# Optimization experiments

Hardware: AMD Instinct MI355X
Metric: run time of the kernel (lower is better)

The kernel has to match this reference:

```python
import jax, jax.numpy as jnp
import numpy as np

B = 8
A = 3
LEVEL_HW = [(200, 304), (100, 152), (50, 76), (25, 38), (13, 19)]
LEVEL_SIZES = [A * h * w for h, w in LEVEL_HW]  # anchors per level
N_TOTAL = sum(LEVEL_SIZES)                      # 242991
IMG_H, IMG_W = 800.0, 1216.0
PRE_NMS_TOP_N = 2000
POST_NMS_TOP_N = 100
NMS_THRESH = 0.7
MIN_SIZE = 1e-3
BBOX_XFORM_CLIP = float(np.log(1000.0 / 16.0))
NEG = -1e30


def setup_inputs() -> dict:
    key = jax.random.key(0)
    ks = jax.random.split(key, 2 * len(LEVEL_HW) + 3)
    inp = {}
    for i, (h, w) in enumerate(LEVEL_HW):
        inp[f"cls{i}"] = jax.random.normal(ks[2 * i], (B, A, h, w), dtype=jnp.float32)
        inp[f"box{i}"] = jax.random.normal(ks[2 * i + 1], (B, 4 * A, h, w), dtype=jnp.float32) * 0.5
    kc, kw, _ = ks[-3], ks[-2], ks[-1]
    c = jax.random.uniform(kc, (N_TOTAL, 2), dtype=jnp.float32) * jnp.array([IMG_W, IMG_H], jnp.float32)
    wh = 16.0 + jax.random.uniform(kw, (N_TOTAL, 2), dtype=jnp.float32) * 240.0
    inp["anchors"] = jnp.concatenate([c - 0.5 * wh, c + 0.5 * wh], axis=-1)  # x1y1x2y2
    return inp


def _permute_flatten(p, C):
    # [N, A*C, H, W] -> [N, H*W*A, C]  (matches permute_and_flatten)
    n, ac, h, w = p.shape
    a = ac // C
    return p.reshape(n, a, C, h, w).transpose(0, 3, 4, 1, 2).reshape(n, -1, C)


def _decode(deltas, anchors):
    wa = anchors[:, 2] - anchors[:, 0]
    ha = anchors[:, 3] - anchors[:, 1]
    cxa = anchors[:, 0] + 0.5 * wa
    cya = anchors[:, 1] + 0.5 * ha
    dx, dy = deltas[..., 0], deltas[..., 1]
    dw = jnp.minimum(deltas[..., 2], BBOX_XFORM_CLIP)
    dh = jnp.minimum(deltas[..., 3], BBOX_XFORM_CLIP)
    cx = dx * wa + cxa
    cy = dy * ha + cya
    pw = jnp.exp(dw) * wa
    ph = jnp.exp(dh) * ha
    return jnp.stack([cx - 0.5 * pw, cy - 0.5 * ph, cx + 0.5 * pw, cy + 0.5 * ph], axis=-1)


def _nms_single(boxes, scores, lvl, valid):
    # batched_nms: offset boxes by level so cross-level boxes never overlap
    off = lvl.astype(boxes.dtype)[:, None] * (max(IMG_H, IMG_W) + 1.0)
    b0 = boxes + off
    s0 = jnp.where(valid, scores, NEG)  # small-box removal -> impossible to pick
    order = jnp.argsort(-s0)
    b = b0[order]
    s = s0[order]
    areas = (b[:, 2] - b[:, 0]) * (b[:, 3] - b[:, 1])
    suppressed0 = s <= NEG / 2
    idx_range = jnp.arange(s.shape[0])

    def step(suppressed, _):
        avail = jnp.where(suppressed, NEG, s)
        i = jnp.argmax(avail)
        ok = avail[i] > NEG / 2
        bi = b[i]
        xx1 = jnp.maximum(b[:, 0], bi[0])
        yy1 = jnp.maximum(b[:, 1], bi[1])
        xx2 = jnp.minimum(b[:, 2], bi[2])
        yy2 = jnp.minimum(b[:, 3], bi[3])
        inter = jnp.maximum(xx2 - xx1, 0.0) * jnp.maximum(yy2 - yy1, 0.0)
        union = areas + areas[i] - inter
        iou = jnp.where(union > 0, inter / union, 0.0)
        sup_new = suppressed | (iou > NMS_THRESH) | (idx_range == i)
        return jnp.where(ok, sup_new, suppressed), (jnp.where(ok, order[i], 0), ok)

    _, (sel, selv) = jax.lax.scan(step, suppressed0, None, length=POST_NMS_TOP_N)
    out_boxes = jnp.where(selv[:, None], boxes[sel], 0.0)
    out_scores = jnp.where(selv, scores[sel], 0.0)
    return out_boxes, out_scores


def reference(cls0, cls1, cls2, cls3, cls4, box0, box1, box2, box3, box4, anchors):
    cls_levels = [cls0, cls1, cls2, cls3, cls4]
    box_levels = [box0, box1, box2, box3, box4]
    pred_class = jnp.concatenate([_permute_flatten(c, 1) for c in cls_levels], axis=1)  # [B,N,1]
    deltas = jnp.concatenate([_permute_flatten(b, 4) for b in box_levels], axis=1)      # [B,N,4]
    proposals = _decode(deltas, anchors)                                               # [B,N,4]
    scores = pred_class[..., 0]                                                        # [B,N]

    # per-level top-k; replicates the original's cumulative k = min(k, num_anchor)
    keep, lvl = [], []
    k, off = PRE_NMS_TOP_N, 0
    for li, n in enumerate(LEVEL_SIZES):
        k = min(k, n)
        _, idx = jax.lax.top_k(scores[:, off:off + n], k)
        keep.append(idx + off)
        lvl.append(jnp.full((k,), li, dtype=jnp.int32))
        off += n
    keep = jnp.concatenate(keep, axis=1)   # [B,K]
    lvl = jnp.concatenate(lvl)             # [K]

    prop = jnp.take_along_axis(proposals, keep[..., None], axis=1)  # [B,K,4]
    sc = jnp.take_along_axis(scores, keep, axis=1)                  # [B,K]
    prop = jnp.stack([
        jnp.clip(prop[..., 0], 0.0, IMG_W), jnp.clip(prop[..., 1], 0.0, IMG_H),
        jnp.clip(prop[..., 2], 0.0, IMG_W), jnp.clip(prop[..., 3], 0.0, IMG_H)], axis=-1)
    valid = ((prop[..., 2] - prop[..., 0]) >= MIN_SIZE) & ((prop[..., 3] - prop[..., 1]) >= MIN_SIZE)
    boxes_out, scores_out = jax.vmap(lambda bx, s, v: _nms_single(bx, s, lvl, v))(prop, sc, valid)
    return boxes_out, scores_out  # [B,100,4], [B,100]
```

## Files before the change

### kernel.cpp

```cpp
#include <hip/hip_runtime.h>
#include <cstdint>

#define NTOT 242991
#define BATCH 8
#define KTOT 8741
#define CAP 8192
#define NBIN 4096
#define CSTR 16
#define MEMTOT 1943928
#define SLICE 256
#define RSTR 9
#define BCAP 2048
#define NB2 2048

__device__ __forceinline__ int level_of(int n) {
    if (n < 182400) return 0;
    if (n < 228000) return 1;
    if (n < 239400) return 2;
    if (n < 242250) return 3;
    return 4;
}

__device__ __forceinline__ void locate(int n, int& l, int& H, int& W, int& loc) {
    if (n < 182400)      { l = 0; H = 200; W = 304; loc = n; }
    else if (n < 228000) { l = 1; H = 100; W = 152; loc = n - 182400; }
    else if (n < 239400) { l = 2; H = 50;  W = 76;  loc = n - 228000; }
    else if (n < 242250) { l = 3; H = 25;  W = 38;  loc = n - 239400; }
    else                 { l = 4; H = 13;  W = 19;  loc = n - 242250; }
}

__device__ __forceinline__ int classify_bl(int x) {
    int l, HW;
    if (x < 1459200)      { l = 0; HW = 60800; }
    else if (x < 1824000) { l = 1; HW = 15200; x -= 1459200; }
    else if (x < 1915200) { l = 2; HW = 3800;  x -= 1824000; }
    else if (x < 1938000) { l = 3; HW = 950;   x -= 1915200; }
    else                  { l = 4; HW = 247;   x -= 1938000; }
    return (x / (3 * HW)) * 5 + l;
}

__device__ __forceinline__ void mem_decompose(int x, int& b, int& n, int& bl) {
    int HW, off, l;
    if (x < 1459200)      { l = 0; HW = 60800; off = 0; }
    else if (x < 1824000) { l = 1; HW = 15200; off = 182400; x -= 1459200; }
    else if (x < 1915200) { l = 2; HW = 3800;  off = 228000; x -= 1824000; }
    else if (x < 1938000) { l = 3; HW = 950;   off = 239400; x -= 1915200; }
    else                  { l = 4; HW = 247;   off = 242250; x -= 1938000; }
    int seg = 3 * HW;
    b = x / seg; int r = x - b * seg;
    int a = r / HW, pix = r - a * HW;
    n = off + pix * 3 + a;
    bl = b * 5 + l;
}

__device__ __forceinline__ float read_cls(int gid, const float* c0, const float* c1,
                                          const float* c2, const float* c3, const float* c4) {
    return (gid < 1459200) ? c0[gid] :
           (gid < 1824000) ? c1[gid - 1459200] :
           (gid < 1915200) ? c2[gid - 1824000] :
           (gid < 1938000) ? c3[gid - 1915200] : c4[gid - 1938000];
}

__device__ __forceinline__ uint32_t suffix_scan_1024(uint32_t g, uint32_t* lds16, int t) {
    int lane = t & 63, wid = t >> 6;
    uint32_t v = g;
#pragma unroll
    for (int o = 1; o < 64; o <<= 1) {
        uint32_t oth = __shfl_down(v, o, 64);
        if (lane + o < 64) v += oth;
    }
    if (lane == 0) lds16[wid] = v;
    __syncthreads();
    uint32_t w = 0;
    for (int q = wid + 1; q < 16; q++) w += lds16[q];
    __syncthreads();
    return v + w;
}

__device__ __forceinline__ unsigned long long suffix_scan64(unsigned long long g,
                                                            unsigned long long* lds64, int t) {
    int lane = t & 63, wid = t >> 6;
    unsigned long long v = g;
#pragma unroll
    for (int o = 1; o < 64; o <<= 1) {
        unsigned long long oth = __shfl_down(v, o, 64);
        if (lane + o < 64) v += oth;
    }
    if (lane == 0) lds64[wid] = v;
    __syncthreads();
    unsigned long long w = 0;
    for (int q = wid + 1; q < 16; q++) w += lds64[q];
    __syncthreads();
    return v + w;
}

__device__ __forceinline__ uint32_t prefix_scan_1024(uint32_t g, uint32_t* lds16, int t) {
    int lane = t & 63, wid = t >> 6;
    uint32_t v = g;
#pragma unroll
    for (int o = 1; o < 64; o <<= 1) {
        uint32_t oth = __shfl_up(v, o, 64);
        if (lane >= o) v += oth;
    }
    if (lane == 63) lds16[wid] = v;
    __syncthreads();
    uint32_t w = 0;
    for (int q = 0; q < wid; q++) w += lds16[q];
    __syncthreads();
    return v + w;
}

__device__ __forceinline__ bool iou_hit(float bx1, float by1, float bx2, float by2, float ca,
                                        float4 sv) {
    float xx1 = fmaxf(bx1, sv.x), yy1 = fmaxf(by1, sv.y);
    float xx2 = fminf(bx2, sv.z), yy2 = fminf(by2, sv.w);
    float inter = fmaxf(xx2 - xx1, 0.f) * fmaxf(yy2 - yy1, 0.f);
    float sa = (sv.z - sv.x) * (sv.w - sv.y);
    float un = ca + sa - inter;
    return (un > 0.f) && (inter / un > 0.7f);
}

__global__ __launch_bounds__(1024)
void k_keys(const float* __restrict__ c0, const float* __restrict__ c1,
            const float* __restrict__ c2, const float* __restrict__ c3,
            const float* __restrict__ c4, uint32_t* __restrict__ hist) {
    int t = threadIdx.x;
    int base = blockIdx.x * 1024;
    int gid = base + t;
    bool in = gid < MEMTOT;
    __shared__ uint32_t lh[NBIN];

    int bl = 0, b, n;
    uint32_t u = 0;
    if (in) {
        mem_decompose(gid, b, n, bl);
        float sv = read_cls(gid, c0, c1, c2, c3, c4);
        u = __float_as_uint(sv);
        u ^= (u >> 31) ? 0xFFFFFFFFu : 0x80000000u;
    }
    int blf = classify_bl(base);
    int bll = classify_bl(min(base + 1023, MEMTOT - 1));
    if (blf == bll) {
        for (int j = t; j < NBIN; j += 1024) lh[j] = 0u;
        __syncthreads();
        if (in) atomicAdd(&lh[u >> 20], 1u);
        __syncthreads();
        uint32_t* gh = hist + (size_t)blf * NBIN;
        for (int j = t; j < NBIN; j += 1024) {
            uint32_t v = lh[j];
            if (v) atomicAdd(&gh[j], v);
        }
    } else {
        if (in) atomicAdd(&hist[(size_t)bl * NBIN + (u >> 20)], 1u);
    }
}

__global__ void k_bins(const uint32_t* __restrict__ hist, int* __restrict__ binT,
                       int* __restrict__ rrem) {
    int bl = blockIdx.x;
    const uint32_t* h = hist + (size_t)bl * NBIN;
    int l = bl % 5;
    uint32_t k = (l == 4) ? 741u : 2000u;
    __shared__ uint32_t ts[256];
    __shared__ uint32_t sb[256];
    int t = threadIdx.x;
    uint32_t hh[16];
#pragma unroll
    for (int i = 0; i < 16; i++) hh[i] = h[t * 16 + i];
    uint32_t s = 0;
#pragma unroll
    for (int i = 0; i < 16; i++) s += hh[i];
    ts[t] = s; sb[t] = s;
    __syncthreads();
    for (int d = 1; d < 256; d <<= 1) {
// ... 82 lines not shown
            if (p < CAP) {
                cand_n[(size_t)bl * CAP + p] = (uint32_t)n;
                cand_u[(size_t)bl * CAP + p] = u;
            }
        }
    }
}

__global__ __launch_bounds__(1024)
void k_select(const uint32_t* __restrict__ cand_n, const uint32_t* __restrict__ cand_u,
              const uint32_t* __restrict__ cand_cnt, const int* __restrict__ rrem,
              uint32_t* __restrict__ keep_n, uint32_t* __restrict__ keep_u,
              uint32_t* __restrict__ keep_cnt) {
    int bl = blockIdx.x;
    int b = bl / 5, l = bl % 5;
    int C = (int)min(cand_cnt[bl * CSTR], (uint32_t)CAP);
    int r = rrem[bl];
    const uint32_t* cdn = cand_n + (size_t)bl * CAP;
    const uint32_t* cdu = cand_u + (size_t)bl * CAP;
    __shared__ uint32_t hist_l[2048];
    __shared__ uint32_t lds16[16];
    __shared__ unsigned long long pref_sh;
    __shared__ uint32_t kk_sh;
    int t = threadIdx.x;
    if (t == 0) { pref_sh = 0ull; kk_sh = (uint32_t)r; }
    unsigned long long maskAcc = 0ull;
    const int shifts[5] = {41, 30, 19, 8, 0};
    const uint32_t masks[5] = {0x7FFu, 0x7FFu, 0x7FFu, 0x7FFu, 0xFFu};
    __syncthreads();
    for (int p = 0; p < 5; p++) {
        int shift = shifts[p];
        uint32_t msk = masks[p];
        for (int j = t; j < 2048; j += 1024) hist_l[j] = 0u;
        __syncthreads();
        unsigned long long pref = pref_sh;
        uint32_t kk = kk_sh;
        for (int i = t; i < C; i += 1024) {
            unsigned long long key =
                ((unsigned long long)cdu[i] << 32) | (uint32_t)(~cdn[i]);
            if ((key & maskAcc) == pref)
                atomicAdd(&hist_l[(uint32_t)(key >> shift) & msk], 1u);
        }
        __syncthreads();
        uint32_t g = hist_l[2 * t] + hist_l[2 * t + 1];
        uint32_t inc = suffix_scan_1024(g, lds16, t);
        uint32_t excl = inc - g;
        if (excl < kk && inc >= kk) {
            uint32_t hh1 = hist_l[2 * t + 1];
            uint32_t digit, rem;
            if (excl + hh1 >= kk) { digit = 2 * t + 1; rem = kk - excl; }
            else { digit = 2 * t; rem = kk - (excl + hh1); }
            pref_sh = pref | ((unsigned long long)digit << shift);
            kk_sh = rem;
        }
        __syncthreads();
        maskAcc |= (unsigned long long)msk << shift;
    }
    unsigned long long Tk = pref_sh;
    __syncthreads();
    int lane = t & 63;
    for (int i0 = 0; i0 < C; i0 += 1024) {
        int i = i0 + t;
        bool in = i < C;
        uint32_t n = in ? cdn[i] : 0u;
        uint32_t u = in ? cdu[i] : 0u;
        unsigned long long key = in ?
            (((unsigned long long)u << 32) | (uint32_t)(~n)) : 0ull;
        bool pr = in && ((key & maskAcc) >= Tk);
        unsigned long long mk = __ballot(pr);
        if (mk) {
            int leader = __ffsll(mk) - 1;
            uint32_t bs = 0;
            if (lane == leader) bs = atomicAdd(&keep_cnt[bl * CSTR], (uint32_t)__popcll(mk));
            bs = __shfl(bs, leader, 64);
            if (pr) {
                uint32_t p = (uint32_t)(b * KTOT + l * 2000) + bs +
                             (uint32_t)__popcll(mk & ((1ull << lane) - 1ull));
                keep_n[p] = n; keep_u[p] = u;
            }
        }
    }
}

__global__ __launch_bounds__(1024)
void k_prep(const float* __restrict__ b0, const float* __restrict__ b1,
            const float* __restrict__ b2, const float* __restrict__ b3,
            const float* __restrict__ b4, const float* __restrict__ anchors,
            const uint32_t* __restrict__ keep_n, const uint32_t* __restrict__ keep_u,
            unsigned long long* __restrict__ skey, float4* __restrict__ sbox,
            uint32_t* __restrict__ nb_start, uint32_t* __restrict__ nb_cnt,
            uint32_t* __restrict__ nb_id, uint32_t* __restrict__ nbcnt) {
    int b = blockIdx.x, t = threadIdx.x;
    __shared__ uint32_t shist_l[NBIN];
    __shared__ uint32_t scur_l[NBIN];
    __shared__ unsigned long long lds64[16];
    for (int j = t; j < NBIN; j += 1024) shist_l[j] = 0u;
    __syncthreads();

    float4 bx[9]; unsigned long long ky[9];
#pragma unroll
    for (int e = 0; e < 9; e++) {
        int i = t + e * 1024;
        ky[e] = 0ull; bx[e] = make_float4(0.f, 0.f, 0.f, 0.f);
        if (i < KTOT) {
            int gid = b * KTOT + i;
            int n = (int)keep_n[gid];
            uint32_t u = keep_u[gid];
            int l, H, W, loc; locate(n, l, H, W, loc);
            int a = loc % 3, hw = loc / 3;
            int w = hw % W, h = hw / W;
            const float* bp = (l == 0) ? b0 : (l == 1) ? b1 : (l == 2) ? b2
                              : (l == 3) ? b3 : b4;
            int HW = H * W;
            int base = ((b * 12 + a * 4) * H + h) * W + w;
            float dx = bp[base], dy = bp[base + HW];
            float dw = bp[base + 2 * HW], dh = bp[base + 3 * HW];
            float ax1 = anchors[4 * n], ay1 = anchors[4 * n + 1];
            float ax2 = anchors[4 * n + 2], ay2 = anchors[4 * n + 3];
            float wa = ax2 - ax1, ha = ay2 - ay1;
            float cxa = ax1 + 0.5f * wa, cya = ay1 + 0.5f * ha;
            const float CLIPV = 4.135166556742356f;
            dw = fminf(dw, CLIPV); dh = fminf(dh, CLIPV);
            float cx = dx * wa + cxa, cy = dy * ha + cya;
            float pw = expf(dw) * wa, ph = expf(dh) * ha;
            float x1 = cx - 0.5f * pw, y1 = cy - 0.5f * ph;
            float x2 = cx + 0.5f * pw, y2 = cy + 0.5f * ph;
            x1 = fminf(fmaxf(x1, 0.f), 1216.f); x2 = fminf(fmaxf(x2, 0.f), 1216.f);
            y1 = fminf(fmaxf(y1, 0.f), 800.f);  y2 = fminf(fmaxf(y2, 0.f), 800.f);
            bool valid = ((x2 - x1) >= 1e-3f) && ((y2 - y1) >= 1e-3f);
            if (valid) {
                float off = (float)l * 1217.0f;
                bx[e] = make_float4(x1 + off, y1 + off, x2 + off, y2 + off);
                ky[e] = ((unsigned long long)u << 32) | (uint32_t)(~n);
                atomicAdd(&shist_l[u >> 20], 1u);
            }
        }
    }
    __syncthreads();
    uint32_t h0 = shist_l[4 * t], h1 = shist_l[4 * t + 1],
             h2 = shist_l[4 * t + 2], h3 = shist_l[4 * t + 3];
#define PK(c) ((unsigned long long)(c) | ((unsigned long long)((c) > 0u) << 32))
    unsigned long long g = PK(h0) + PK(h1) + PK(h2) + PK(h3);
    unsigned long long inc = suffix_scan64(g, lds64, t);
    unsigned long long acc = inc - g;
    uint32_t* NBS = nb_start + (size_t)b * NBIN;
    uint32_t* NBC = nb_cnt + (size_t)b * NBIN;
    uint32_t* NBI = nb_id + (size_t)b * NBIN;
#define EMIT(q, cq) { int bin = 4 * t + (q); uint32_t st = (uint32_t)acc;            \
                      uint32_t fp = (uint32_t)(acc >> 32);                           \
                      scur_l[bin] = st;                                              \
                      if (cq) { NBS[fp] = st; NBC[fp] = cq; NBI[fp] = (uint32_t)bin; } \
                      acc += PK(cq); }
    EMIT(3, h3) EMIT(2, h2) EMIT(1, h1) EMIT(0, h0)
#undef EMIT
#undef PK
    if (t == 0) nbcnt[b] = (uint32_t)(inc >> 32);
    __syncthreads();
#pragma unroll
    for (int e = 0; e < 9; e++) {
        if (ky[e] != 0ull) {
            uint32_t bucket = (uint32_t)(ky[e] >> 52);
            uint32_t p = atomicAdd(&scur_l[bucket], 1u);
            skey[(size_t)b * KTOT + p] = ky[e];
            sbox[(size_t)b * KTOT + p] = bx[e];
        }
    }
}

__global__ __launch_bounds__(1024)
void k_scan(const unsigned long long* __restrict__ skey, const float4* __restrict__ sbox,
            const uint32_t* __restrict__ nb_start, const uint32_t* __restrict__ nb_cnt,
            const uint32_t* __restrict__ nb_id, const uint32_t* __restrict__ nbcnt,
            float* __restrict__ out) {
    int b = blockIdx.x, t = threadIdx.x, lane = t & 63, wid = t >> 6;
    const unsigned long long* SK = skey + (size_t)b * KTOT;
    const float4* BXs = sbox + (size_t)b * KTOT;
    const uint32_t* NBS = nb_start + (size_t)b * NBIN;
    const uint32_t* NBC = nb_cnt + (size_t)b * NBIN;
    const uint32_t* NBI = nb_id + (size_t)b * NBIN;

    __shared__ unsigned long long k_l[BCAP];
    __shared__ unsigned short p_l[BCAP];
    __shared__ uint32_t hist2[NB2];
    __shared__ uint32_t scur2[NB2];
    __shared__ unsigned char rnk[NBIN];
    __shared__ float box_x[SLICE], box_y[SLICE], box_z[SLICE], box_w[SLICE];
    __shared__ uint32_t rows[SLICE * RSTR];
    __shared__ float4 sel_l[100];
    __shared__ uint32_t sup[SLICE / 32];
    __shared__ uint32_t lds16[16];
    __shared__ uint32_t picks_sh;
    __shared__ unsigned long long gmax_sh;
    __shared__ uint32_t jpos_sh;
    __shared__ unsigned long long wred[16];

    uint32_t nbc = nbcnt[b];
    uint32_t picks = 0;
    uint32_t e = 0;
    while (e < nbc && picks < 100u) {
        uint32_t bstart = NBS[e];
        uint32_t total = 0, nb = 0;
        while (e + nb < nbc && nb < 8u) {
            uint32_t c = NBC[e + nb];
            if (nb > 0u && total + c > (uint32_t)BCAP) break;
            total += c; nb++;
            if (total >= (uint32_t)BCAP) break;
        }

        if (total <= (uint32_t)BCAP) {
            if (t < (int)nb) rnk[NBI[e + t]] = (unsigned char)t;
            for (int j2 = t; j2 < NB2; j2 += 1024) hist2[j2] = 0u;
            __syncthreads();
            unsigned long long k0 = 0ull, k1 = 0ull;
            uint32_t bin0 = 0xFFFFFFFFu, bin1 = 0xFFFFFFFFu;
            if ((uint32_t)t < total) {
                k0 = SK[bstart + (uint32_t)t];
                bin0 = ((uint32_t)rnk[(uint32_t)(k0 >> 52)] << 8) |
                       (255u - (uint32_t)((k0 >> 44) & 0xFFull));
                atomicAdd(&hist2[bin0], 1u);
            }
            if ((uint32_t)t + 1024u < total) {
                k1 = SK[bstart + (uint32_t)t + 1024u];
                bin1 = ((uint32_t)rnk[(uint32_t)(k1 >> 52)] << 8) |
                       (255u - (uint32_t)((k1 >> 44) & 0xFFull));
                atomicAdd(&hist2[bin1], 1u);
            }
            __syncthreads();
            uint32_t h0 = hist2[2 * t], h1 = hist2[2 * t + 1];
            uint32_t inc = prefix_scan_1024(h0 + h1, lds16, t);
            uint32_t excl = inc - (h0 + h1);
            scur2[2 * t] = excl; scur2[2 * t + 1] = excl + h0;
            __syncthreads();
            if (bin0 != 0xFFFFFFFFu) {
                uint32_t pos = atomicAdd(&scur2[bin0], 1u);
                k_l[pos] = k0; p_l[pos] = (unsigned short)(bstart + (uint32_t)t);
            }
            if (bin1 != 0xFFFFFFFFu) {
                uint32_t pos = atomicAdd(&scur2[bin1], 1u);
                k_l[pos] = k1; p_l[pos] = (unsigned short)(bstart + (uint32_t)t + 1024u);
            }
            __syncthreads();
#pragma unroll
            for (int q = 0; q < 2; q++) {
                uint32_t bin = 2 * (uint32_t)t + (uint32_t)q;
                uint32_t c = hist2[bin];
                if (c > 1u) {
                    uint32_t st = scur2[bin] - c;
                    for (uint32_t a = st + 1; a < st + c; a++) {
                        unsigned long long kv = k_l[a]; unsigned short pv = p_l[a];
                        uint32_t w2 = a;
                        while (w2 > st && k_l[w2 - 1] < kv) {
                            k_l[w2] = k_l[w2 - 1]; p_l[w2] = p_l[w2 - 1]; w2--;
                        }
                        k_l[w2] = kv; p_l[w2] = pv;
                    }
                }
            }
            __syncthreads();

            for (uint32_t s0 = 0; s0 < total && picks < 100u; s0 += SLICE) {
                uint32_t sl = min((uint32_t)SLICE, total - s0);
                if (t < SLICE) {
                    if (t < (int)sl) {
                        float4 cb = BXs[p_l[s0 + t]];
                        box_x[t] = cb.x; box_y[t] = cb.y; box_z[t] = cb.z; box_w[t] = cb.w;
                    } else {
                        box_x[t] = 0.f; box_y[t] = 0.f; box_z[t] = 0.f; box_w[t] = 0.f;
                    }
                }
                if (t < SLICE / 32) sup[t] = 0u;
                __syncthreads();
                if (picks > 0u && t < (int)sl) {
                    float bx1 = box_x[t], by1 = box_y[t], bx2 = box_z[t], by2 = box_w[t];
                    float ca = (bx2 - bx1) * (by2 - by1);
                    bool hit = false;
                    uint32_t s = 0;
                    for (; s + 4 <= picks; s += 4) {
                        float4 v0 = sel_l[s], v1 = sel_l[s + 1], v2 = sel_l[s + 2],
                               v3 = sel_l[s + 3];
                        hit = hit | iou_hit(bx1, by1, bx2, by2, ca, v0)
                                  | iou_hit(bx1, by1, bx2, by2, ca, v1)
                                  | iou_hit(bx1, by1, bx2, by2, ca, v2)
                                  | iou_hit(bx1, by1, bx2, by2, ca, v3);
                    }
                    for (; s < picks; s++) hit = hit | iou_hit(bx1, by1, bx2, by2, ca, sel_l[s]);
                    if (hit) atomicOr(&sup[t >> 5], 1u << (t & 31));
                }
                for (uint32_t widx = t; widx < SLICE * 8; widx += 1024) {
                    uint32_t i = widx & (SLICE - 1);
                    uint32_t wq = widx >> 8;
                    float bx1 = box_x[i], by1 = box_y[i], bx2 = box_z[i], by2 = box_w[i];
                    float ai = (bx2 - bx1) * (by2 - by1);
                    uint32_t jbase = wq * 32u, bits = 0u;
#pragma unroll
                    for (uint32_t qq = 0; qq < 32u; qq++) {
                        uint32_t jj = jbase + qq;
                        float jx1 = box_x[jj], jy1 = box_y[jj],
                              jx2 = box_z[jj], jy2 = box_w[jj];
                        float xx1 = fmaxf(bx1, jx1), yy1 = fmaxf(by1, jy1);
                        float xx2 = fminf(bx2, jx2), yy2 = fminf(by2, jy2);
                        float inter = fmaxf(xx2 - xx1, 0.f) * fmaxf(yy2 - yy1, 0.f);
                        float aj = (jx2 - jx1) * (jy2 - jy1);
                        float un = ai + aj - inter;
                        bool sp = (jj > i) && (un > 0.f) && (inter / un > 0.7f);
                        bits |= ((uint32_t)sp) << qq;
                    }
                    rows[i * RSTR + wq] = bits;
                }
                __syncthreads();
                if (wid == 0) {
                    uint32_t myw = (lane < SLICE / 32) ? sup[lane] : 0u;
                    uint32_t pk = picks;
                    for (uint32_t i = 0; i < sl && pk < 100u; i++) {
                        uint32_t wv = __shfl(myw, (int)(i >> 5), 64);
                        if (!((wv >> (i & 31)) & 1u)) {
                            if (lane < SLICE / 32) myw |= rows[i * RSTR + lane];
                            if (lane == 0) {
                                float4 cb = make_float4(box_x[i], box_y[i], box_z[i], box_w[i]);
                                sel_l[pk] = cb;
                                unsigned long long mkey = k_l[s0 + i];
                                uint32_t n = ~(uint32_t)(mkey & 0xFFFFFFFFull);
                                float off = (float)level_of((int)n) * 1217.0f;
                                float* ob = out + ((size_t)b * 100 + pk) * 4;
                                ob[0] = cb.x - off; ob[1] = cb.y - off;
                                ob[2] = cb.z - off; ob[3] = cb.w - off;
                                uint32_t uu = (uint32_t)(mkey >> 32);
                                uint32_t sb2 = (uu & 0x80000000u) ? (uu ^ 0x80000000u) : ~uu;
                                out[3200 + b * 100 + pk] = __uint_as_float(sb2);
                            }
                            pk++;
                        }
                    }
                    if (lane == 0) picks_sh = pk;
                }
                __syncthreads();
                picks = picks_sh;
            }
        } else {
            unsigned long long last = 0ull;
            bool first = true;
            for (uint32_t done = 0; done < total && picks < 100u; done++) {
                unsigned long long lbest = 0ull;
                uint32_t jbest = 0;
                for (uint32_t jj = bstart + t; jj < bstart + total; jj += 1024) {
                    unsigned long long kk = SK[jj];
                    if ((first || kk < last) && kk > lbest) { lbest = kk; jbest = jj; }
                }
                unsigned long long wm = lbest;
#pragma unroll
                for (int o2 = 32; o2 > 0; o2 >>= 1) {
                    unsigned long long oth = __shfl_down(wm, o2, 64);
                    if (oth > wm) wm = oth;
                }
                if (lane == 0) wred[wid] = wm;
                __syncthreads();
                if (t == 0) {
                    unsigned long long mm = wred[0];
                    for (int q = 1; q < 16; q++) if (wred[q] > mm) mm = wred[q];
                    gmax_sh = mm;
                }
                __syncthreads();
                unsigned long long gm = gmax_sh;
                if (gm == 0ull) break;
                if (lbest == gm) jpos_sh = jbest;
                __syncthreads();
                float4 cb = BXs[jpos_sh];
                float ca = (cb.z - cb.x) * (cb.w - cb.y);
                bool hit = false;
                for (uint32_t s = (uint32_t)lane; s < picks; s += 64u)
                    hit = hit | iou_hit(cb.x, cb.y, cb.z, cb.w, ca, sel_l[s]);
                bool selq = (__ballot(hit) == 0ull);
                if (selq) {
                    if (t == 0) {
                        sel_l[picks] = cb;
                        uint32_t n = ~(uint32_t)(gm & 0xFFFFFFFFull);
                        float off = (float)level_of((int)n) * 1217.0f;
                        float* ob = out + ((size_t)b * 100 + picks) * 4;
                        ob[0] = cb.x - off; ob[1] = cb.y - off;
                        ob[2] = cb.z - off; ob[3] = cb.w - off;
                        uint32_t uu = (uint32_t)(gm >> 32);
                        uint32_t sb2 = (uu & 0x80000000u) ? (uu ^ 0x80000000u) : ~uu;
                        out[3200 + b * 100 + picks] = __uint_as_float(sb2);
                    }
                    picks++;
                }
                last = gm; first = false;
                __syncthreads();
            }
        }
        e += nb;
    }
    for (uint32_t i = picks + (uint32_t)t; i < 100u; i += 1024u) {
        float* ob = out + ((size_t)b * 100 + i) * 4;
        ob[0] = 0.f; ob[1] = 0.f; ob[2] = 0.f; ob[3] = 0.f;
        out[3200 + b * 100 + i] = 0.f;
    }
}

extern "C" void kernel_launch(void* const* d_in, const int* in_sizes, int n_in,
                              void* d_out, int out_size, void* d_ws, size_t ws_size,
                              hipStream_t stream) {
    const float* cls[5] = { (const float*)d_in[0], (const float*)d_in[2], (const float*)d_in[4],
                            (const float*)d_in[6], (const float*)d_in[8] };
    const float* box[5] = { (const float*)d_in[1], (const float*)d_in[3], (const float*)d_in[5],
                            (const float*)d_in[7], (const float*)d_in[9] };
    const float* anchors = (const float*)d_in[10];
    float* out = (float*)d_out;

    uint32_t* W32 = (uint32_t*)d_ws;
    size_t o = 0;
    uint32_t* hist     = W32 + o; o += (size_t)40 * NBIN;
    uint32_t* keep_cnt = W32 + o; o += 40 * CSTR;
    uint32_t* cand_cnt = W32 + o; o += 40 * CSTR;
    size_t zero_n = o;
    int*      binT     = (int*)(W32 + o); o += 64;
    int*      rrem     = (int*)(W32 + o); o += 64;
    uint32_t* nbcnt    = W32 + o; o += 16;
    uint32_t* nb_start = W32 + o; o += (size_t)BATCH * NBIN;
    uint32_t* nb_cnt   = W32 + o; o += (size_t)BATCH * NBIN;
    uint32_t* nb_id    = W32 + o; o += (size_t)BATCH * NBIN;
    uint32_t* keep_n   = W32 + o; o += (size_t)BATCH * KTOT;
    uint32_t* keep_u   = W32 + o; o += (size_t)BATCH * KTOT;
    uint32_t* cand_n   = W32 + o; o += (size_t)40 * CAP;
    uint32_t* cand_u   = W32 + o; o += (size_t)40 * CAP;
    o = (o + 3) & ~(size_t)3;
    float4* sbox = (float4*)(W32 + o); o += (size_t)BATCH * KTOT * 4;
    unsigned long long* skey = (unsigned long long*)(W32 + o); o += (size_t)BATCH * KTOT * 2;

    hipMemsetAsync(d_ws, 0, zero_n * sizeof(uint32_t), stream);
    k_keys<<<(MEMTOT + 1023) / 1024, 1024, 0, stream>>>(cls[0], cls[1], cls[2], cls[3], cls[4],
                                                        hist);
    k_bins<<<40, 256, 0, stream>>>(hist, binT, rrem);
    k_compact<<<(MEMTOT + 1023) / 1024, 1024, 0, stream>>>(cls[0], cls[1], cls[2], cls[3],
                                                           cls[4], binT, keep_n, keep_u,
                                                           keep_cnt, cand_n, cand_u, cand_cnt);
    k_select<<<40, 1024, 0, stream>>>(cand_n, cand_u, cand_cnt, rrem, keep_n, keep_u, keep_cnt);
    k_prep<<<BATCH, 1024, 0, stream>>>(box[0], box[1], box[2], box[3], box[4], anchors,
                                       keep_n, keep_u, skey, sbox,
                                       nb_start, nb_cnt, nb_id, nbcnt);
    k_scan<<<BATCH, 1024, 0, stream>>>(skey, sbox, nb_start, nb_cnt, nb_id, nbcnt, out);
}
```

Baseline: 160.9 us.

## Split per-batch prep into grid-wide decode, bucket scan and scatter kernels

The single-block-per-batch prep kernel, which decoded boxes, built a bucket histogram, scanned it and scattered keys, is replaced by three kernels. A grid-wide decode kernel computes boxes and keys and builds the histogram with global atomics. A small scan kernel computes bucket offsets, and a grid-wide scatter places keys and boxes. The aim is to spread the latency-bound gather and decode over many workgroups instead of only 8. In exchange it adds two kernel launches, intermediate global buffers and global atomics.

```diff
diff --git a/kernel.cpp b/kernel.cpp
--- a/kernel.cpp
+++ b/kernel.cpp
@@ -338,89 +338,84 @@
     }
 }
 
+__global__ void k_decode(const float* __restrict__ b0, const float* __restrict__ b1,
+                         const float* __restrict__ b2, const float* __restrict__ b3,
+                         const float* __restrict__ b4, const float* __restrict__ anchors,
+                         const uint32_t* __restrict__ keep_n, const uint32_t* __restrict__ keep_u,
+                         float4* __restrict__ nbox, unsigned long long* __restrict__ nkey,
+                         uint32_t* __restrict__ shist) {
+    int gid = blockIdx.x * blockDim.x + threadIdx.x;
+    if (gid >= BATCH * KTOT) return;
+    int b = gid / KTOT;
+    int n = (int)keep_n[gid];
+    uint32_t u = keep_u[gid];
+    int l, H, W, loc; locate(n, l, H, W, loc);
+    int a = loc % 3, hw = loc / 3;
+    int w = hw % W, h = hw / W;
+    const float* bp = (l == 0) ? b0 : (l == 1) ? b1 : (l == 2) ? b2 : (l == 3) ? b3 : b4;
+    int HW = H * W;
+    int base = ((b * 12 + a * 4) * H + h) * W + w;
+    float dx = bp[base], dy = bp[base + HW];
+    float dw = bp[base + 2 * HW], dh = bp[base + 3 * HW];
+    float ax1 = anchors[4 * n], ay1 = anchors[4 * n + 1];
+    float ax2 = anchors[4 * n + 2], ay2 = anchors[4 * n + 3];
+    float wa = ax2 - ax1, ha = ay2 - ay1;
+    float cxa = ax1 + 0.5f * wa, cya = ay1 + 0.5f * ha;
+    const float CLIPV = 4.135166556742356f;
+    dw = fminf(dw, CLIPV); dh = fminf(dh, CLIPV);
+    float cx = dx * wa + cxa, cy = dy * ha + cya;
+    float pw = expf(dw) * wa, ph = expf(dh) * ha;
+    float x1 = cx - 0.5f * pw, y1 = cy - 0.5f * ph;
+    float x2 = cx + 0.5f * pw, y2 = cy + 0.5f * ph;
+    x1 = fminf(fmaxf(x1, 0.f), 1216.f); x2 = fminf(fmaxf(x2, 0.f), 1216.f);
+    y1 = fminf(fmaxf(y1, 0.f), 800.f);  y2 = fminf(fmaxf(y2, 0.f), 800.f);
+    bool valid = ((x2 - x1) >= 1e-3f) && ((y2 - y1) >= 1e-3f);
+    float off = (float)l * 1217.0f;
+    nbox[gid] = make_float4(x1 + off, y1 + off, x2 + off, y2 + off);
+    nkey[gid] = valid ? (((unsigned long long)u << 32) | (uint32_t)(~n)) : 0ull;
+    if (valid) atomicAdd(&shist[b * NBIN + (u >> 20)], 1u);
+}
+
 __global__ __launch_bounds__(1024)
-void k_prep(const float* __restrict__ b0, const float* __restrict__ b1,
-            const float* __restrict__ b2, const float* __restrict__ b3,
-            const float* __restrict__ b4, const float* __restrict__ anchors,
-            const uint32_t* __restrict__ keep_n, const uint32_t* __restrict__ keep_u,
-            unsigned long long* __restrict__ skey, float4* __restrict__ sbox,
-            uint32_t* __restrict__ nb_start, uint32_t* __restrict__ nb_cnt,
-            uint32_t* __restrict__ nb_id, uint32_t* __restrict__ nbcnt) {
+void k_scanbuckets(const uint32_t* __restrict__ shist, uint32_t* __restrict__ scursor,
+                   uint32_t* __restrict__ nb_start, uint32_t* __restrict__ nb_cnt,
+                   uint32_t* __restrict__ nb_id, uint32_t* __restrict__ nbcnt) {
     int b = blockIdx.x, t = threadIdx.x;
-    __shared__ uint32_t shist_l[NBIN];
-    __shared__ uint32_t scur_l[NBIN];
+    const uint32_t* h = shist + (size_t)b * NBIN;
     __shared__ unsigned long long lds64[16];
-    for (int j = t; j < NBIN; j += 1024) shist_l[j] = 0u;
-    __syncthreads();
-
-    float4 bx[9]; unsigned long long ky[9];
-#pragma unroll
-    for (int e = 0; e < 9; e++) {
-        int i = t + e * 1024;
-        ky[e] = 0ull; bx[e] = make_float4(0.f, 0.f, 0.f, 0.f);
-        if (i < KTOT) {
-            int gid = b * KTOT + i;
-            int n = (int)keep_n[gid];
-            uint32_t u = keep_u[gid];
-            int l, H, W, loc; locate(n, l, H, W, loc);
-            int a = loc % 3, hw = loc / 3;
-            int w = hw % W, h = hw / W;
-            const float* bp = (l == 0) ? b0 : (l == 1) ? b1 : (l == 2) ? b2
-                              : (l == 3) ? b3 : b4;
-            int HW = H * W;
-            int base = ((b * 12 + a * 4) * H + h) * W + w;
-            float dx = bp[base], dy = bp[base + HW];
-            float dw = bp[base + 2 * HW], dh = bp[base + 3 * HW];
-            float ax1 = anchors[4 * n], ay1 = anchors[4 * n + 1];
-            float ax2 = anchors[4 * n + 2], ay2 = anchors[4 * n + 3];
-            float wa = ax2 - ax1, ha = ay2 - ay1;
-            float cxa = ax1 + 0.5f * wa, cya = ay1 + 0.5f * ha;
-            const float CLIPV = 4.135166556742356f;
-            dw = fminf(dw, CLIPV); dh = fminf(dh, CLIPV);
-            float cx = dx * wa + cxa, cy = dy * ha + cya;
-            float pw = expf(dw) * wa, ph = expf(dh) * ha;
-            float x1 = cx - 0.5f * pw, y1 = cy - 0.5f * ph;
-            float x2 = cx + 0.5f * pw, y2 = cy + 0.5f * ph;
-            x1 = fminf(fmaxf(x1, 0.f), 1216.f); x2 = fminf(fmaxf(x2, 0.f), 1216.f);
-            y1 = fminf(fmaxf(y1, 0.f), 800.f);  y2 = fminf(fmaxf(y2, 0.f), 800.f);
-            bool valid = ((x2 - x1) >= 1e-3f) && ((y2 - y1) >= 1e-3f);
-            if (valid) {
-                float off = (float)l * 1217.0f;
-                bx[e] = make_float4(x1 + off, y1 + off, x2 + off, y2 + off);
-                ky[e] = ((unsigned long long)u << 32) | (uint32_t)(~n);
-                atomicAdd(&shist_l[u >> 20], 1u);
-            }
-        }
-    }
-    __syncthreads();
-    uint32_t h0 = shist_l[4 * t], h1 = shist_l[4 * t + 1],
-             h2 = shist_l[4 * t + 2], h3 = shist_l[4 * t + 3];
+    uint32_t h0 = h[4 * t], h1 = h[4 * t + 1], h2 = h[4 * t + 2], h3 = h[4 * t + 3];
 #define PK(c) ((unsigned long long)(c) | ((unsigned long long)((c) > 0u) << 32))
     unsigned long long g = PK(h0) + PK(h1) + PK(h2) + PK(h3);
     unsigned long long inc = suffix_scan64(g, lds64, t);
     unsigned long long acc = inc - g;
+    uint32_t* SC = scursor + (size_t)b * NBIN;
     uint32_t* NBS = nb_start + (size_t)b * NBIN;
     uint32_t* NBC = nb_cnt + (size_t)b * NBIN;
     uint32_t* NBI = nb_id + (size_t)b * NBIN;
 #define EMIT(q, cq) { int bin = 4 * t + (q); uint32_t st = (uint32_t)acc;            \
                       uint32_t fp = (uint32_t)(acc >> 32);                           \
-                      scur_l[bin] = st;                                              \
+                      SC[bin] = st;                                                  \
                       if (cq) { NBS[fp] = st; NBC[fp] = cq; NBI[fp] = (uint32_t)bin; } \
                       acc += PK(cq); }
     EMIT(3, h3) EMIT(2, h2) EMIT(1, h1) EMIT(0, h0)
 #undef EMIT
 #undef PK
     if (t == 0) nbcnt[b] = (uint32_t)(inc >> 32);
-    __syncthreads();
-#pragma unroll
-    for (int e = 0; e < 9; e++) {
-        if (ky[e] != 0ull) {
-            uint32_t bucket = (uint32_t)(ky[e] >> 52);
-            uint32_t p = atomicAdd(&scur_l[bucket], 1u);
-            skey[(size_t)b * KTOT + p] = ky[e];
-            sbox[(size_t)b * KTOT + p] = bx[e];
-        }
-    }
+}
+
+__global__ void k_scatter(const unsigned long long* __restrict__ nkey,
+                          const float4* __restrict__ nbox,
+                          uint32_t* __restrict__ scursor,
+                          unsigned long long* __restrict__ skey, float4* __restrict__ sbox) {
+    int gid = blockIdx.x * blockDim.x + threadIdx.x;
+    if (gid >= BATCH * KTOT) return;
+    unsigned long long kk = nkey[gid];
+    if (kk == 0ull) return;
+    int b = gid / KTOT;
+    uint32_t bucket = (uint32_t)(kk >> 52);
+    uint32_t p = atomicAdd(&scursor[b * NBIN + bucket], 1u);
+    skey[(size_t)b * KTOT + p] = kk;
+    sbox[(size_t)b * KTOT + p] = nbox[gid];
 }
 
 __global__ __launch_bounds__(1024)
@@ -666,12 +661,14 @@
     uint32_t* W32 = (uint32_t*)d_ws;
     size_t o = 0;
     uint32_t* hist     = W32 + o; o += (size_t)40 * NBIN;
+    uint32_t* shist    = W32 + o; o += (size_t)BATCH * NBIN;
     uint32_t* keep_cnt = W32 + o; o += 40 * CSTR;
     uint32_t* cand_cnt = W32 + o; o += 40 * CSTR;
     size_t zero_n = o;
     int*      binT     = (int*)(W32 + o); o += 64;
     int*      rrem     = (int*)(W32 + o); o += 64;
     uint32_t* nbcnt    = W32 + o; o += 16;
+    uint32_t* scursor  = W32 + o; o += (size_t)BATCH * NBIN;
     uint32_t* nb_start = W32 + o; o += (size_t)BATCH * NBIN;
     uint32_t* nb_cnt   = W32 + o; o += (size_t)BATCH * NBIN;
     uint32_t* nb_id    = W32 + o; o += (size_t)BATCH * NBIN;
@@ -680,6 +677,8 @@
     uint32_t* cand_n   = W32 + o; o += (size_t)40 * CAP;
     uint32_t* cand_u   = W32 + o; o += (size_t)40 * CAP;
     o = (o + 3) & ~(size_t)3;
+    float4* nbox = (float4*)(W32 + o); o += (size_t)BATCH * KTOT * 4;
+    unsigned long long* nkey = (unsigned long long*)(W32 + o); o += (size_t)BATCH * KTOT * 2;
     float4* sbox = (float4*)(W32 + o); o += (size_t)BATCH * KTOT * 4;
     unsigned long long* skey = (unsigned long long*)(W32 + o); o += (size_t)BATCH * KTOT * 2;
 
@@ -691,8 +690,16 @@
                                                            cls[4], binT, keep_n, keep_u,
                                                            keep_cnt, cand_n, cand_u, cand_cnt);
     k_select<<<40, 1024, 0, stream>>>(cand_n, cand_u, cand_cnt, rrem, keep_n, keep_u, keep_cnt);
-    k_prep<<<BATCH, 1024, 0, stream>>>(box[0], box[1], box[2], box[3], box[4], anchors,
-                                       keep_n, keep_u, skey, sbox,
-                                       nb_start, nb_cnt, nb_id, nbcnt);
+    {
+        int tot = BATCH * KTOT;
+        k_decode<<<(tot + 255) / 256, 256, 0, stream>>>(box[0], box[1], box[2], box[3], box[4],
+                                                        anchors, keep_n, keep_u,
+                                                        nbox, nkey, shist);
+    }
+    k_scanbuckets<<<BATCH, 1024, 0, stream>>>(shist, scursor, nb_start, nb_cnt, nb_id, nbcnt);
+    {
+        int tot = BATCH * KTOT;
+        k_scatter<<<(tot + 255) / 256, 256, 0, stream>>>(nkey, nbox, scursor, skey, sbox);
+    }
     k_scan<<<BATCH, 1024, 0, stream>>>(skey, sbox, nb_start, nb_cnt, nb_id, nbcnt, out);
 }
```

Result: slower. 194.4 us (+20.8%).

## Split box decode across more blocks and move bucket scatter into NMS kernel

Applied to the files above, without the earlier changes.

Box decoding and the coarse score histogram now run in a separate kernel with 9 blocks per image instead of one, and the per-image histograms are merged with global atomics. The histogram scan and the bucket scatter move into the NMS kernel. The NMS kernel now forms its chunks by a score-position range instead of a bin list, and sub-bins are sized in proportion to each bucket's count. Shared memory is reused across phases to cut LDS footprint. The aim is to spread the latency-bound gather and decode over many more CUs, at the cost of an extra global round trip for the decoded boxes and keys, plus an additional scatter pass inside the serial NMS block.

```diff
diff --git a/kernel.cpp b/kernel.cpp
--- a/kernel.cpp
+++ b/kernel.cpp
@@ -12,6 +12,7 @@
 #define RSTR 9
 #define BCAP 2048
 #define NB2 2048
+#define DBLK 9
 
 __device__ __forceinline__ int level_of(int n) {
     if (n < 182400) return 0;
@@ -73,23 +74,6 @@
     __syncthreads();
     uint32_t w = 0;
     for (int q = wid + 1; q < 16; q++) w += lds16[q];
-    __syncthreads();
-    return v + w;
-}
-
-__device__ __forceinline__ unsigned long long suffix_scan64(unsigned long long g,
-                                                            unsigned long long* lds64, int t) {
-    int lane = t & 63, wid = t >> 6;
-    unsigned long long v = g;
-#pragma unroll
-    for (int o = 1; o < 64; o <<= 1) {
-        unsigned long long oth = __shfl_down(v, o, 64);
-        if (lane + o < 64) v += oth;
-    }
-    if (lane == 0) lds64[wid] = v;
-    __syncthreads();
-    unsigned long long w = 0;
-    for (int q = wid + 1; q < 16; q++) w += lds64[q];
     __syncthreads();
     return v + w;
 }
@@ -339,166 +323,173 @@
 }
 
 __global__ __launch_bounds__(1024)
-void k_prep(const float* __restrict__ b0, const float* __restrict__ b1,
-            const float* __restrict__ b2, const float* __restrict__ b3,
-            const float* __restrict__ b4, const float* __restrict__ anchors,
-            const uint32_t* __restrict__ keep_n, const uint32_t* __restrict__ keep_u,
-            unsigned long long* __restrict__ skey, float4* __restrict__ sbox,
-            uint32_t* __restrict__ nb_start, uint32_t* __restrict__ nb_cnt,
-            uint32_t* __restrict__ nb_id, uint32_t* __restrict__ nbcnt) {
-    int b = blockIdx.x, t = threadIdx.x;
-    __shared__ uint32_t shist_l[NBIN];
-    __shared__ uint32_t scur_l[NBIN];
-    __shared__ unsigned long long lds64[16];
-    for (int j = t; j < NBIN; j += 1024) shist_l[j] = 0u;
-    __syncthreads();
-
-    float4 bx[9]; unsigned long long ky[9];
-#pragma unroll
-    for (int e = 0; e < 9; e++) {
-        int i = t + e * 1024;
-        ky[e] = 0ull; bx[e] = make_float4(0.f, 0.f, 0.f, 0.f);
-        if (i < KTOT) {
-            int gid = b * KTOT + i;
-            int n = (int)keep_n[gid];
-            uint32_t u = keep_u[gid];
-            int l, H, W, loc; locate(n, l, H, W, loc);
-            int a = loc % 3, hw = loc / 3;
-            int w = hw % W, h = hw / W;
-            const float* bp = (l == 0) ? b0 : (l == 1) ? b1 : (l == 2) ? b2
-                              : (l == 3) ? b3 : b4;
-            int HW = H * W;
-            int base = ((b * 12 + a * 4) * H + h) * W + w;
-            float dx = bp[base], dy = bp[base + HW];
-            float dw = bp[base + 2 * HW], dh = bp[base + 3 * HW];
-            float ax1 = anchors[4 * n], ay1 = anchors[4 * n + 1];
-            float ax2 = anchors[4 * n + 2], ay2 = anchors[4 * n + 3];
-            float wa = ax2 - ax1, ha = ay2 - ay1;
-            float cxa = ax1 + 0.5f * wa, cya = ay1 + 0.5f * ha;
-            const float CLIPV = 4.135166556742356f;
-            dw = fminf(dw, CLIPV); dh = fminf(dh, CLIPV);
-            float cx = dx * wa + cxa, cy = dy * ha + cya;
-            float pw = expf(dw) * wa, ph = expf(dh) * ha;
-            float x1 = cx - 0.5f * pw, y1 = cy - 0.5f * ph;
-            float x2 = cx + 0.5f * pw, y2 = cy + 0.5f * ph;
-            x1 = fminf(fmaxf(x1, 0.f), 1216.f); x2 = fminf(fmaxf(x2, 0.f), 1216.f);
-            y1 = fminf(fmaxf(y1, 0.f), 800.f);  y2 = fminf(fmaxf(y2, 0.f), 800.f);
-            bool valid = ((x2 - x1) >= 1e-3f) && ((y2 - y1) >= 1e-3f);
-            if (valid) {
-                float off = (float)l * 1217.0f;
-                bx[e] = make_float4(x1 + off, y1 + off, x2 + off, y2 + off);
-                ky[e] = ((unsigned long long)u << 32) | (uint32_t)(~n);
-                atomicAdd(&shist_l[u >> 20], 1u);
-            }
-        }
-    }
-    __syncthreads();
-    uint32_t h0 = shist_l[4 * t], h1 = shist_l[4 * t + 1],
-             h2 = shist_l[4 * t + 2], h3 = shist_l[4 * t + 3];
-#define PK(c) ((unsigned long long)(c) | ((unsigned long long)((c) > 0u) << 32))
-    unsigned long long g = PK(h0) + PK(h1) + PK(h2) + PK(h3);
-    unsigned long long inc = suffix_scan64(g, lds64, t);
-    unsigned long long acc = inc - g;
-    uint32_t* NBS = nb_start + (size_t)b * NBIN;
-    uint32_t* NBC = nb_cnt + (size_t)b * NBIN;
-    uint32_t* NBI = nb_id + (size_t)b * NBIN;
-#define EMIT(q, cq) { int bin = 4 * t + (q); uint32_t st = (uint32_t)acc;            \
-                      uint32_t fp = (uint32_t)(acc >> 32);                           \
-                      scur_l[bin] = st;                                              \
-                      if (cq) { NBS[fp] = st; NBC[fp] = cq; NBI[fp] = (uint32_t)bin; } \
-                      acc += PK(cq); }
-    EMIT(3, h3) EMIT(2, h2) EMIT(1, h1) EMIT(0, h0)
-#undef EMIT
-#undef PK
-    if (t == 0) nbcnt[b] = (uint32_t)(inc >> 32);
-    __syncthreads();
-#pragma unroll
-    for (int e = 0; e < 9; e++) {
-        if (ky[e] != 0ull) {
-            uint32_t bucket = (uint32_t)(ky[e] >> 52);
-            uint32_t p = atomicAdd(&scur_l[bucket], 1u);
-            skey[(size_t)b * KTOT + p] = ky[e];
-            sbox[(size_t)b * KTOT + p] = bx[e];
-        }
+void k_decode(const float* __restrict__ b0, const float* __restrict__ b1,
+              const float* __restrict__ b2, const float* __restrict__ b3,
+              const float* __restrict__ b4, const float* __restrict__ anchors,
+              const uint32_t* __restrict__ keep_n, const uint32_t* __restrict__ keep_u,
+              float4* __restrict__ nbox, unsigned long long* __restrict__ nkey,
+              uint32_t* __restrict__ shist) {
+    int blk = blockIdx.x;
+    int b = blk / DBLK, seg = blk % DBLK;
+    int i = seg * 1024 + threadIdx.x;
+    int t = threadIdx.x;
+    __shared__ uint32_t lh[NBIN];
+    for (int j = t; j < NBIN; j += 1024) lh[j] = 0u;
+    __syncthreads();
+    if (i < KTOT) {
+        int gid = b * KTOT + i;
+        int n = (int)keep_n[gid];
+        uint32_t u = keep_u[gid];
+        int l, H, W, loc; locate(n, l, H, W, loc);
+        int a = loc % 3, hw = loc / 3;
+        int w = hw % W, h = hw / W;
+        const float* bp = (l == 0) ? b0 : (l == 1) ? b1 : (l == 2) ? b2 : (l == 3) ? b3 : b4;
+        int HW = H * W;
+        int base = ((b * 12 + a * 4) * H + h) * W + w;
+        float dx = bp[base], dy = bp[base + HW];
+        float dw = bp[base + 2 * HW], dh = bp[base + 3 * HW];
+        float ax1 = anchors[4 * n], ay1 = anchors[4 * n + 1];
+        float ax2 = anchors[4 * n + 2], ay2 = anchors[4 * n + 3];
+        float wa = ax2 - ax1, ha = ay2 - ay1;
+        float cxa = ax1 + 0.5f * wa, cya = ay1 + 0.5f * ha;
+        const float CLIPV = 4.135166556742356f;
+        dw = fminf(dw, CLIPV); dh = fminf(dh, CLIPV);
+        float cx = dx * wa + cxa, cy = dy * ha + cya;
+        float pw = expf(dw) * wa, ph = expf(dh) * ha;
+        float x1 = cx - 0.5f * pw, y1 = cy - 0.5f * ph;
+        float x2 = cx + 0.5f * pw, y2 = cy + 0.5f * ph;
+        x1 = fminf(fmaxf(x1, 0.f), 1216.f); x2 = fminf(fmaxf(x2, 0.f), 1216.f);
+        y1 = fminf(fmaxf(y1, 0.f), 800.f);  y2 = fminf(fmaxf(y2, 0.f), 800.f);
+        bool valid = ((x2 - x1) >= 1e-3f) && ((y2 - y1) >= 1e-3f);
+        float off = (float)l * 1217.0f;
+        nbox[gid] = make_float4(x1 + off, y1 + off, x2 + off, y2 + off);
+        nkey[gid] = valid ? (((unsigned long long)u << 32) | (uint32_t)(~n)) : 0ull;
+        if (valid) atomicAdd(&lh[u >> 20], 1u);
+    }
+    __syncthreads();
+    uint32_t* gh = shist + (size_t)b * NBIN;
+    for (int j = t; j < NBIN; j += 1024) {
+        uint32_t v = lh[j];
+        if (v) atomicAdd(&gh[j], v);
     }
 }
 
 __global__ __launch_bounds__(1024)
-void k_scan(const unsigned long long* __restrict__ skey, const float4* __restrict__ sbox,
-            const uint32_t* __restrict__ nb_start, const uint32_t* __restrict__ nb_cnt,
-            const uint32_t* __restrict__ nb_id, const uint32_t* __restrict__ nbcnt,
-            float* __restrict__ out) {
+void k_nms(const unsigned long long* __restrict__ nkey, const float4* __restrict__ nbox,
+           const uint32_t* __restrict__ shist,
+           unsigned long long* __restrict__ skey, float4* __restrict__ sbox,
+           float* __restrict__ out) {
     int b = blockIdx.x, t = threadIdx.x, lane = t & 63, wid = t >> 6;
-    const unsigned long long* SK = skey + (size_t)b * KTOT;
-    const float4* BXs = sbox + (size_t)b * KTOT;
-    const uint32_t* NBS = nb_start + (size_t)b * NBIN;
-    const uint32_t* NBC = nb_cnt + (size_t)b * NBIN;
-    const uint32_t* NBI = nb_id + (size_t)b * NBIN;
-
+    unsigned long long* SK = skey + (size_t)b * KTOT;
+    float4* BXs = sbox + (size_t)b * KTOT;
+
+    __shared__ unsigned short bstart16[NBIN];
+    __shared__ unsigned short bcnt16[NBIN];
     __shared__ unsigned long long k_l[BCAP];
     __shared__ unsigned short p_l[BCAP];
-    __shared__ uint32_t hist2[NB2];
-    __shared__ uint32_t scur2[NB2];
-    __shared__ unsigned char rnk[NBIN];
-    __shared__ float box_x[SLICE], box_y[SLICE], box_z[SLICE], box_w[SLICE];
-    __shared__ uint32_t rows[SLICE * RSTR];
+    __shared__ uint32_t scratch[4096];
     __shared__ float4 sel_l[100];
     __shared__ uint32_t sup[SLICE / 32];
     __shared__ uint32_t lds16[16];
-    __shared__ uint32_t picks_sh;
+    __shared__ uint32_t V_sh, picks_sh, bend_sh, fat_sh;
     __shared__ unsigned long long gmax_sh;
     __shared__ uint32_t jpos_sh;
     __shared__ unsigned long long wred[16];
 
-    uint32_t nbc = nbcnt[b];
+    const uint32_t* H = shist + (size_t)b * NBIN;
+    uint32_t h0 = H[4 * t], h1 = H[4 * t + 1], h2 = H[4 * t + 2], h3 = H[4 * t + 3];
+    uint32_t g = h0 + h1 + h2 + h3;
+    uint32_t inc = suffix_scan_1024(g, lds16, t);
+    if (t == 0) { V_sh = inc; picks_sh = 0u; }
+    uint32_t acc = inc - g;
+    uint32_t* scur32 = scratch;
+    bstart16[4 * t + 3] = (unsigned short)acc; bcnt16[4 * t + 3] = (unsigned short)h3;
+    scur32[4 * t + 3] = acc; acc += h3;
+    bstart16[4 * t + 2] = (unsigned short)acc; bcnt16[4 * t + 2] = (unsigned short)h2;
+    scur32[4 * t + 2] = acc; acc += h2;
+    bstart16[4 * t + 1] = (unsigned short)acc; bcnt16[4 * t + 1] = (unsigned short)h1;
+    scur32[4 * t + 1] = acc; acc += h1;
+    bstart16[4 * t + 0] = (unsigned short)acc; bcnt16[4 * t + 0] = (unsigned short)h0;
+    scur32[4 * t + 0] = acc;
+    __syncthreads();
+
+#pragma unroll
+    for (int e = 0; e < DBLK; e++) {
+        int i = t + e * 1024;
+        if (i < KTOT) {
+            unsigned long long kk = nkey[(size_t)b * KTOT + i];
+            if (kk != 0ull) {
+                uint32_t q = (uint32_t)(kk >> 52);
+                uint32_t p = atomicAdd(&scur32[q], 1u);
+                SK[p] = kk;
+                BXs[p] = nbox[(size_t)b * KTOT + i];
+            }
+        }
+    }
+    __threadfence();
+    __syncthreads();
+
+    uint32_t V = V_sh;
     uint32_t picks = 0;
-    uint32_t e = 0;
-    while (e < nbc && picks < 100u) {
-        uint32_t bstart = NBS[e];
-        uint32_t total = 0, nb = 0;
-        while (e + nb < nbc && nb < 8u) {
-            uint32_t c = NBC[e + nb];
-            if (nb > 0u && total + c > (uint32_t)BCAP) break;
-            total += c; nb++;
-            if (total >= (uint32_t)BCAP) break;
-        }
-
-        if (total <= (uint32_t)BCAP) {
-            if (t < (int)nb) rnk[NBI[e + t]] = (unsigned char)t;
-            for (int j2 = t; j2 < NB2; j2 += 1024) hist2[j2] = 0u;
+    uint32_t P = 0;
+    while (P < V && picks < 100u) {
+        uint32_t target = min(P + (uint32_t)BCAP, V);
+        if (t == 0) { bend_sh = P; fat_sh = P; }
+        __syncthreads();
+        for (int q = t; q < NBIN; q += 1024) {
+            uint32_t c = bcnt16[q];
+            if (c) {
+                uint32_t s = bstart16[q];
+                if (s >= P && s + c <= target) atomicMax(&bend_sh, s + c);
+                if (s == P) fat_sh = P + c;
+            }
+        }
+        __syncthreads();
+        uint32_t B = bend_sh;
+
+        if (B > P) {
+            uint32_t total = B - P;
+            uint32_t* hist2 = scratch;
+            uint32_t* scur2 = scratch + 2048;
+            for (int j = t; j < NB2; j += 1024) hist2[j] = 0u;
             __syncthreads();
             unsigned long long k0 = 0ull, k1 = 0ull;
             uint32_t bin0 = 0xFFFFFFFFu, bin1 = 0xFFFFFFFFu;
-            if ((uint32_t)t < total) {
-                k0 = SK[bstart + (uint32_t)t];
-                bin0 = ((uint32_t)rnk[(uint32_t)(k0 >> 52)] << 8) |
-                       (255u - (uint32_t)((k0 >> 44) & 0xFFull));
+            uint32_t j0 = P + (uint32_t)t, j1 = P + (uint32_t)t + 1024u;
+            if (j0 < B) {
+                k0 = SK[j0];
+                uint32_t q = (uint32_t)(k0 >> 52);
+                uint32_t c = bcnt16[q], rel = (uint32_t)bstart16[q] - P;
+                uint32_t sub = (uint32_t)((k0 >> 44) & 0xFFull);
+                bin0 = rel + ((c * (255u - sub)) >> 8);
                 atomicAdd(&hist2[bin0], 1u);
             }
-            if ((uint32_t)t + 1024u < total) {
-                k1 = SK[bstart + (uint32_t)t + 1024u];
-                bin1 = ((uint32_t)rnk[(uint32_t)(k1 >> 52)] << 8) |
-                       (255u - (uint32_t)((k1 >> 44) & 0xFFull));
+            if (j1 < B) {
+                k1 = SK[j1];
+                uint32_t q = (uint32_t)(k1 >> 52);
+                uint32_t c = bcnt16[q], rel = (uint32_t)bstart16[q] - P;
+                uint32_t sub = (uint32_t)((k1 >> 44) & 0xFFull);
+                bin1 = rel + ((c * (255u - sub)) >> 8);
                 atomicAdd(&hist2[bin1], 1u);
             }
             __syncthreads();
-            uint32_t h0 = hist2[2 * t], h1 = hist2[2 * t + 1];
-            uint32_t inc = prefix_scan_1024(h0 + h1, lds16, t);
-            uint32_t excl = inc - (h0 + h1);
-            scur2[2 * t] = excl; scur2[2 * t + 1] = excl + h0;
+            uint32_t g0 = hist2[2 * t], g1 = hist2[2 * t + 1];
+            uint32_t incp = prefix_scan_1024(g0 + g1, lds16, t);
+            uint32_t excl = incp - (g0 + g1);
+            scur2[2 * t] = excl; scur2[2 * t + 1] = excl + g0;
             __syncthreads();
             if (bin0 != 0xFFFFFFFFu) {
                 uint32_t pos = atomicAdd(&scur2[bin0], 1u);
-                k_l[pos] = k0; p_l[pos] = (unsigned short)(bstart + (uint32_t)t);
+                k_l[pos] = k0; p_l[pos] = (unsigned short)j0;
             }
             if (bin1 != 0xFFFFFFFFu) {
                 uint32_t pos = atomicAdd(&scur2[bin1], 1u);
-                k_l[pos] = k1; p_l[pos] = (unsigned short)(bstart + (uint32_t)t + 1024u);
+                k_l[pos] = k1; p_l[pos] = (unsigned short)j1;
             }
             __syncthreads();
 #pragma unroll
-            for (int q = 0; q < 2; q++) {
-                uint32_t bin = 2 * (uint32_t)t + (uint32_t)q;
+            for (int qq = 0; qq < 2; qq++) {
+                uint32_t bin = 2 * (uint32_t)t + (uint32_t)qq;
                 uint32_t c = hist2[bin];
                 if (c > 1u) {
                     uint32_t st = scur2[bin] - c;
@@ -514,8 +505,14 @@
             }
             __syncthreads();
 
+            float* box_x = (float*)scratch;
+            float* box_y = box_x + SLICE;
+            float* box_z = box_y + SLICE;
+            float* box_w = box_z + SLICE;
+            uint32_t* rows = scratch + 1024;
             for (uint32_t s0 = 0; s0 < total && picks < 100u; s0 += SLICE) {
                 uint32_t sl = min((uint32_t)SLICE, total - s0);
+                __syncthreads();
                 if (t < SLICE) {
                     if (t < (int)sl) {
                         float4 cb = BXs[p_l[s0 + t]];
@@ -592,13 +589,16 @@
                 __syncthreads();
                 picks = picks_sh;
             }
+            __syncthreads();
         } else {
+            B = fat_sh;
+            uint32_t cnt = B - P;
             unsigned long long last = 0ull;
             bool first = true;
-            for (uint32_t done = 0; done < total && picks < 100u; done++) {
+            for (uint32_t done = 0; done < cnt && picks < 100u; done++) {
                 unsigned long long lbest = 0ull;
                 uint32_t jbest = 0;
-                for (uint32_t jj = bstart + t; jj < bstart + total; jj += 1024) {
+                for (uint32_t jj = P + t; jj < B; jj += 1024) {
                     unsigned long long kk = SK[jj];
                     if ((first || kk < last) && kk > lbest) { lbest = kk; jbest = jj; }
                 }
@@ -644,7 +644,8 @@
                 __syncthreads();
             }
         }
-        e += nb;
+        P = B;
+        __syncthreads();
     }
     for (uint32_t i = picks + (uint32_t)t; i < 100u; i += 1024u) {
         float* ob = out + ((size_t)b * 100 + i) * 4;
@@ -666,20 +667,19 @@
     uint32_t* W32 = (uint32_t*)d_ws;
     size_t o = 0;
     uint32_t* hist     = W32 + o; o += (size_t)40 * NBIN;
+    uint32_t* shist    = W32 + o; o += (size_t)BATCH * NBIN;
     uint32_t* keep_cnt = W32 + o; o += 40 * CSTR;
     uint32_t* cand_cnt = W32 + o; o += 40 * CSTR;
     size_t zero_n = o;
     int*      binT     = (int*)(W32 + o); o += 64;
     int*      rrem     = (int*)(W32 + o); o += 64;
-    uint32_t* nbcnt    = W32 + o; o += 16;
-    uint32_t* nb_start = W32 + o; o += (size_t)BATCH * NBIN;
-    uint32_t* nb_cnt   = W32 + o; o += (size_t)BATCH * NBIN;
-    uint32_t* nb_id    = W32 + o; o += (size_t)BATCH * NBIN;
     uint32_t* keep_n   = W32 + o; o += (size_t)BATCH * KTOT;
     uint32_t* keep_u   = W32 + o; o += (size_t)BATCH * KTOT;
     uint32_t* cand_n   = W32 + o; o += (size_t)40 * CAP;
     uint32_t* cand_u   = W32 + o; o += (size_t)40 * CAP;
     o = (o + 3) & ~(size_t)3;
+    float4* nbox = (float4*)(W32 + o); o += (size_t)BATCH * KTOT * 4;
+    unsigned long long* nkey = (unsigned long long*)(W32 + o); o += (size_t)BATCH * KTOT * 2;
     float4* sbox = (float4*)(W32 + o); o += (size_t)BATCH * KTOT * 4;
     unsigned long long* skey = (unsigned long long*)(W32 + o); o += (size_t)BATCH * KTOT * 2;
 
@@ -691,8 +691,7 @@
                                                            cls[4], binT, keep_n, keep_u,
                                                            keep_cnt, cand_n, cand_u, cand_cnt);
     k_select<<<40, 1024, 0, stream>>>(cand_n, cand_u, cand_cnt, rrem, keep_n, keep_u, keep_cnt);
-    k_prep<<<BATCH, 1024, 0, stream>>>(box[0], box[1], box[2], box[3], box[4], anchors,
-                                       keep_n, keep_u, skey, sbox,
-                                       nb_start, nb_cnt, nb_id, nbcnt);
-    k_scan<<<BATCH, 1024, 0, stream>>>(skey, sbox, nb_start, nb_cnt, nb_id, nbcnt, out);
-}
+    k_decode<<<BATCH * DBLK, 1024, 0, stream>>>(box[0], box[1], box[2], box[3], box[4],
+                                                anchors, keep_n, keep_u, nbox, nkey, shist);
+    k_nms<<<BATCH, 1024, 0, stream>>>(nkey, nbox, shist, skey, sbox, out);
+}
```

Measured after the change: 147.8 us. -8.1%, faster.
